# Performance work log

Measured on AMD Instinct MI355X. Metric: run time of the kernel, lower is better.

Reference implementation:

```python
import jax, jax.numpy as jnp
import numpy as np

N = 100000   # nodes
E = 1600000  # edges
D = 128      # input / hidden feature dim
H = 16       # inner GCN bottleneck (gin default hidden_filters=(16,))
C = 40       # num_classes (ogbn-arxiv)
L = 3        # GCN2 layers
EPS = 1e-5   # hk.BatchNorm default eps


def setup_inputs() -> dict:
    key = jax.random.key(0)
    ks = jax.random.split(key, 8)
    x = jax.random.normal(ks[0], (N, D), jnp.float32)
    vals = jax.random.uniform(ks[1], (E,), jnp.float32)
    row = jnp.sort(jax.random.randint(ks[2], (E,), 0, N, jnp.int32))
    col = jax.random.randint(ks[3], (E,), 0, N, jnp.int32)
    W1 = jax.random.normal(ks[4], (L, D, H), jnp.float32) * 0.1
    b1 = jnp.zeros((L, H), jnp.float32)
    W2 = jax.random.normal(ks[5], (L, H, D), jnp.float32) * 0.1
    b2 = jnp.zeros((L, D), jnp.float32)
    gamma = jnp.ones((L, D), jnp.float32)
    beta = jnp.zeros((L, D), jnp.float32)
    W1f = jax.random.normal(ks[6], (D, H), jnp.float32) * 0.1
    b1f = jnp.zeros((H,), jnp.float32)
    W2f = jax.random.normal(ks[7], (H, C), jnp.float32) * 0.1
    b2f = jnp.zeros((C,), jnp.float32)
    return dict(x=x, vals=vals, W1=W1, b1=b1, W2=W2, b2=b2, gamma=gamma,
                beta=beta, W1f=W1f, b1f=b1f, W2f=W2f, b2f=b2f, row=row, col=col)


def spmm(row, col, vals, h):
    # out[i] = sum_{e: row[e]==i} vals[e] * h[col[e]]  (A @ h, A sparse COO)
    return jax.ops.segment_sum(vals[:, None] * h[col], row,
                               num_segments=N, indices_are_sorted=True)


def gcn_block(x, row, col, vals, w1, c1, w2, c2):
    # inner GCN: GraphConv(16) -> relu -> GraphConv(out); dropout_rate=0 -> identity
    h = spmm(row, col, vals, x @ w1) + c1
    h = jax.nn.relu(h)
    return spmm(row, col, vals, h @ w2) + c2


def reference(x, vals, W1, b1, W2, b2, gamma, beta, W1f, b1f, W2f, b2f, row, col):
    for i in range(L):
        h = gcn_block(x, row, col, vals, W1[i], b1[i], W2[i], b2[i])
        # BatchNorm (training mode: batch stats over node axis)
        mean = jnp.mean(h, axis=0)
        var = jnp.mean(jnp.square(h), axis=0) - jnp.square(mean)
        h = (h - mean) * jax.lax.rsqrt(var + EPS) * gamma[i] + beta[i]
        x = jax.nn.relu(h)
    logits = gcn_block(x, row, col, vals, W1f, b1f, W2f, b2f)
    return logits
```

## Files before the change

kernel.cpp:

```cpp
#include <hip/hip_runtime.h>

#define NN 100000
#define NE 1600000
#define DD 128
#define HH 16
#define CC 40
#define LL 3

typedef int   vi4 __attribute__((ext_vector_type(4)));
typedef float vf4 __attribute__((ext_vector_type(4)));

__device__ __forceinline__ float4 f4fma(float s, float4 w, float4 a) {
    a.x = fmaf(s, w.x, a.x); a.y = fmaf(s, w.y, a.y);
    a.z = fmaf(s, w.z, a.z); a.w = fmaf(s, w.w, a.w);
    return a;
}

__device__ __forceinline__ unsigned short f2bf(float f) {
    unsigned u = __float_as_uint(f);
    unsigned r = u + 0x7fffu + ((u >> 16) & 1u);
    return (unsigned short)(r >> 16);
}
__device__ __forceinline__ unsigned pk2(float a, float b) {
    return (unsigned)f2bf(a) | ((unsigned)f2bf(b) << 16);
}
__device__ __forceinline__ float bflo(unsigned u) { return __uint_as_float(u << 16); }
__device__ __forceinline__ float bfhi(unsigned u) { return __uint_as_float(u & 0xffff0000u); }

__device__ __forceinline__ int permW2(int dw) {
    return (dw >> 2) | ((dw & 3) << 3);
}

__global__ void build_rowptr(const int* __restrict__ row, int* __restrict__ rp) {
    int e = blockIdx.x * 256 + threadIdx.x;
    if (e >= NE) return;
    int r1 = row[e];
    int r0 = (e == 0) ? -1 : row[e - 1];
    for (int i = r0 + 1; i <= r1; i++) rp[i] = e;
    if (e == NE - 1) {
        for (int i = r1 + 1; i <= NN; i++) rp[i] = NE;
    }
}

__global__ void zero_buf(float* __restrict__ s, int n) {
    int i = blockIdx.x * 256 + threadIdx.x;
    if (i < n) s[i] = 0.f;
}

__launch_bounds__(256)
__global__ void gemm_dh_reg(const float* __restrict__ X, const float* __restrict__ W,
                            unsigned* __restrict__ Y) {
    __shared__ float4 Ws[DD * 4];
    int t = threadIdx.x;
    for (int i = t; i < DD * 4; i += 256) Ws[i] = ((const float4*)W)[i];
    __syncthreads();
    int n = blockIdx.x * 256 + t;
    if (n >= NN) return;
    const float4* X4 = (const float4*)(X + (size_t)n * DD);
    float4 y0 = {0,0,0,0}, y1 = {0,0,0,0}, y2 = {0,0,0,0}, y3 = {0,0,0,0};
    #pragma unroll 8
    for (int dc = 0; dc < 32; dc++) {
        float4 xv = X4[dc];
        float xs[4] = {xv.x, xv.y, xv.z, xv.w};
        #pragma unroll
        for (int j = 0; j < 4; j++) {
            int d = dc * 4 + j;
            float xj = xs[j];
            y0 = f4fma(xj, Ws[d * 4 + 0], y0);
            y1 = f4fma(xj, Ws[d * 4 + 1], y1);
            y2 = f4fma(xj, Ws[d * 4 + 2], y2);
            y3 = f4fma(xj, Ws[d * 4 + 3], y3);
        }
    }
    uint4 o0 = {pk2(y0.x, y0.y), pk2(y0.z, y0.w), pk2(y1.x, y1.y), pk2(y1.z, y1.w)};
    uint4 o1 = {pk2(y2.x, y2.y), pk2(y2.z, y2.w), pk2(y3.x, y3.y), pk2(y3.z, y3.w)};
    ((uint4*)Y)[(size_t)n * 2]     = o0;
    ((uint4*)Y)[(size_t)n * 2 + 1] = o1;
}

#define FMA_B(vv, g0, g1, g2, g3)                                                      \
    acc.x = fmaf(vv.x, bflo(g0.x), acc.x); acc.y = fmaf(vv.x, bfhi(g0.x), acc.y);      \
    acc.z = fmaf(vv.x, bflo(g0.y), acc.z); acc.w = fmaf(vv.x, bfhi(g0.y), acc.w);      \
    acc.x = fmaf(vv.y, bflo(g1.x), acc.x); acc.y = fmaf(vv.y, bfhi(g1.x), acc.y);      \
    acc.z = fmaf(vv.y, bflo(g1.y), acc.z); acc.w = fmaf(vv.y, bfhi(g1.y), acc.w);      \
    acc.x = fmaf(vv.z, bflo(g2.x), acc.x); acc.y = fmaf(vv.z, bfhi(g2.x), acc.y);      \
    acc.z = fmaf(vv.z, bflo(g2.y), acc.z); acc.w = fmaf(vv.z, bfhi(g2.y), acc.w);      \
    acc.x = fmaf(vv.w, bflo(g3.x), acc.x); acc.y = fmaf(vv.w, bfhi(g3.x), acc.y);      \
    acc.z = fmaf(vv.w, bflo(g3.y), acc.z); acc.w = fmaf(vv.w, bfhi(g3.y), acc.w);

template <bool RELU, bool BIAS, bool OBF, bool GRAM>
__launch_bounds__(256)
__global__ void spmm16(const int* __restrict__ rp, const int* __restrict__ col,
                       const float* __restrict__ vals, const unsigned* __restrict__ hin,
                       const float* __restrict__ bias, void* __restrict__ outv,
                       float* __restrict__ GS) {
    int node = blockIdx.x * 64 + (threadIdx.x >> 2);
    int f = threadIdx.x & 3;
    bool valid = node < NN;
    if (!GRAM && !valid) return;
    float4 acc = {0, 0, 0, 0};
    if (valid) {
        int s = rp[node], e = rp[node + 1];
        const uint2* h2 = (const uint2*)hin;
        int j = s;
        int sa = min((s + 3) & ~3, e);
        for (; j < sa; j++) {
            uint2 g = h2[(size_t)col[j] * 4 + f];
            float v = vals[j];
            acc.x = fmaf(v, bflo(g.x), acc.x); acc.y = fmaf(v, bfhi(g.x), acc.y);
            acc.z = fmaf(v, bflo(g.y), acc.z); acc.w = fmaf(v, bfhi(g.y), acc.w);
        }
        int nb = (e - j) >> 2;
        if (nb >= 2) {
            vi4 cA = __builtin_nontemporal_load((const vi4*)(col + j));
            vf4 vA = __builtin_nontemporal_load((const vf4*)(vals + j));
            vi4 cB = __builtin_nontemporal_load((const vi4*)(col + j + 4));
            vf4 vB = __builtin_nontemporal_load((const vf4*)(vals + j + 4));
            uint2 gA0 = h2[(size_t)cA.x * 4 + f];
            uint2 gA1 = h2[(size_t)cA.y * 4 + f];
            uint2 gA2 = h2[(size_t)cA.z * 4 + f];
            uint2 gA3 = h2[(size_t)cA.w * 4 + f];
            int jj = j + 8;
            j += nb << 2;
            for (int r = nb - 2; r > 0; r--) {
                vi4 cC = __builtin_nontemporal_load((const vi4*)(col + jj));
                vf4 vC = __builtin_nontemporal_load((const vf4*)(vals + jj));
                uint2 gB0 = h2[(size_t)cB.x * 4 + f];
                uint2 gB1 = h2[(size_t)cB.y * 4 + f];
                uint2 gB2 = h2[(size_t)cB.z * 4 + f];
                uint2 gB3 = h2[(size_t)cB.w * 4 + f];
                FMA_B(vA, gA0, gA1, gA2, gA3)
                vA = vB; vB = vC; cB = cC;
                gA0 = gB0; gA1 = gB1; gA2 = gB2; gA3 = gB3;
                jj += 4;
            }
            uint2 gB0 = h2[(size_t)cB.x * 4 + f];
            uint2 gB1 = h2[(size_t)cB.y * 4 + f];
            uint2 gB2 = h2[(size_t)cB.z * 4 + f];
            uint2 gB3 = h2[(size_t)cB.w * 4 + f];
            FMA_B(vA, gA0, gA1, gA2, gA3)
            FMA_B(vB, gB0, gB1, gB2, gB3)
        } else if (nb == 1) {
            vi4 cA = __builtin_nontemporal_load((const vi4*)(col + j));
            vf4 vA = __builtin_nontemporal_load((const vf4*)(vals + j));
            uint2 gA0 = h2[(size_t)cA.x * 4 + f];
            uint2 gA1 = h2[(size_t)cA.y * 4 + f];
            uint2 gA2 = h2[(size_t)cA.z * 4 + f];
            uint2 gA3 = h2[(size_t)cA.w * 4 + f];
            FMA_B(vA, gA0, gA1, gA2, gA3)
            j += 4;
        }
        for (; j < e; j++) {
            uint2 g = h2[(size_t)col[j] * 4 + f];
            float v = vals[j];
            acc.x = fmaf(v, bflo(g.x), acc.x); acc.y = fmaf(v, bfhi(g.x), acc.y);
            acc.z = fmaf(v, bflo(g.y), acc.z); acc.w = fmaf(v, bfhi(g.y), acc.w);
        }
        if (BIAS) {
            float4 b = ((const float4*)bias)[f];
            acc.x += b.x; acc.y += b.y; acc.z += b.z; acc.w += b.w;
        }
        if (RELU) {
            acc.x = fmaxf(acc.x, 0.f); acc.y = fmaxf(acc.y, 0.f);
            acc.z = fmaxf(acc.z, 0.f); acc.w = fmaxf(acc.w, 0.f);
        }
        if (OBF) {
            uint2 o = {pk2(acc.x, acc.y), pk2(acc.z, acc.w)};
            ((uint2*)outv)[(size_t)node * 4 + f] = o;
        } else {
            ((float4*)outv)[(size_t)node * 4 + f] = acc;
        }
    }
    if (GRAM) {
        __shared__ float Us[64 * 20];
        int nl = threadIdx.x >> 2;
        float4 z = valid ? acc : (float4){0, 0, 0, 0};
        ((float4*)&Us[nl * 20])[f] = z;
        __syncthreads();
        int k = threadIdx.x & 15, kp = threadIdx.x >> 4;
        float g = 0.f, s = 0.f;
        for (int n = 0; n < 64; n++) {
            float a = Us[n * 20 + k];
            float b = Us[n * 20 + kp];
            g = fmaf(a, b, g);
            s += a;
        }
        float* gs = GS + (blockIdx.x & 7) * 272;
        atomicAdd(&gs[kp * 16 + k], g);
        if (kp == 0) atomicAdd(&gs[256 + k], s);
    }
}

__launch_bounds__(128)
__global__ void bn_prep(const float* __restrict__ GS, const float* __restrict__ W2,
                        const float* __restrict__ b2, const float* __restrict__ gamma,
                        const float* __restrict__ beta, float* __restrict__ SCSH) {
    __shared__ float Gs[272];
    int t = threadIdx.x;
    for (int i = t; i < 272; i += 128) {
        float a = 0.f;
        #pragma unroll
        for (int c = 0; c < 8; c++) a += GS[c * 272 + i];
        Gs[i] = a;
    }
    __syncthreads();
    int d = t;
    float w[16];
    #pragma unroll
    for (int k = 0; k < 16; k++) w[k] = W2[k * DD + d];
    float sdot = 0.f, quad = 0.f;
    #pragma unroll
    for (int k = 0; k < 16; k++) {
        sdot = fmaf(Gs[256 + k], w[k], sdot);
        float vk = 0.f;
        #pragma unroll
        for (int kp = 0; kp < 16; kp++) vk = fmaf(Gs[k * 16 + kp], w[kp], vk);
        quad = fmaf(w[k], vk, quad);
    }
    float b = b2[d];
    float sumH  = sdot + (float)NN * b;
    float sumsq = quad + 2.f * b * sdot + (float)NN * b * b;
    float mean = sumH * (1.f / NN);
    float var  = sumsq * (1.f / NN) - mean * mean;
    float inv  = rsqrtf(var + 1e-5f);
    float gm = gamma[d] * inv;
    SCSH[d] = gm;
    SCSH[128 + d] = (b - mean) * gm + beta[d];
}

__launch_bounds__(256)
__global__ void fused_mid(const float* __restrict__ U, const float* __restrict__ SCSH,
                          const float* __restrict__ W2, const float* __restrict__ W1n,
                          unsigned* __restrict__ Y) {
    __shared__ float4 W2s[HH * 32];
    __shared__ float4 W1s[DD * 4];
    __shared__ float4 SC4[32], SH4[32];
    int t = threadIdx.x;
    for (int i = t; i < HH * 32; i += 256) {
        int k = i >> 5, dw = i & 31;
        W2s[k * 32 + permW2(dw)] = ((const float4*)W2)[i];
    }
    for (int i = t; i < DD * 4; i += 256) {
        int d = i >> 2, q = i & 3;
        W1s[d * 4 + ((q + (d >> 4)) & 3)] = ((const float4*)W1n)[i];
    }
    if (t < 32) SC4[permW2(t)] = ((const float4*)SCSH)[t];
    else if (t < 64) SH4[permW2(t - 32)] = ((const float4*)SCSH)[t];
    __syncthreads();
    int g = t >> 3, p = t & 7;
    int base = blockIdx.x * 64;
    int n[2]; bool v[2];
    #pragma unroll
    for (int i = 0; i < 2; i++) { n[i] = base + i * 32 + g; v[i] = n[i] < NN; }
    float u[2][16];
    #pragma unroll
    for (int i = 0; i < 2; i++) {
        if (v[i]) {
            const float4* up = (const float4*)(U + (size_t)n[i] * HH);
            float4 a = up[0], b = up[1], c = up[2], d = up[3];
            u[i][0]=a.x; u[i][1]=a.y; u[i][2]=a.z; u[i][3]=a.w;
            u[i][4]=b.x; u[i][5]=b.y; u[i][6]=b.z; u[i][7]=b.w;
            u[i][8]=c.x; u[i][9]=c.y; u[i][10]=c.z; u[i][11]=c.w;
            u[i][12]=d.x; u[i][13]=d.y; u[i][14]=d.z; u[i][15]=d.w;
        } else {
            #pragma unroll
            for (int k = 0; k < 16; k++) u[i][k] = 0.f;
        }
    }
    float4 y[2][4];
    #pragma unroll
    for (int i = 0; i < 2; i++)
        #pragma unroll
        for (int q = 0; q < 4; q++) y[i][q] = {0, 0, 0, 0};
    #pragma unroll
    for (int dqi = 0; dqi < 4; dqi++) {
        int rpos = p + (dqi << 3);
        float4 h[2] = {{0,0,0,0},{0,0,0,0}};
        #pragma unroll
        for (int k = 0; k < 16; k++) {
            float4 w = W2s[k * 32 + rpos];
            h[0] = f4fma(u[0][k], w, h[0]);
            h[1] = f4fma(u[1][k], w, h[1]);
        }
        float4 s4 = SC4[rpos], t4 = SH4[rpos];
        #pragma unroll
        for (int i = 0; i < 2; i++) {
            h[i].x = fmaxf(fmaf(h[i].x, s4.x, t4.x), 0.f);
            h[i].y = fmaxf(fmaf(h[i].y, s4.y, t4.y), 0.f);
            h[i].z = fmaxf(fmaf(h[i].z, s4.z, t4.z), 0.f);
            h[i].w = fmaxf(fmaf(h[i].w, s4.w, t4.w), 0.f);
        }
        int dq = (p << 2) + dqi;
        #pragma unroll
        for (int j = 0; j < 4; j++) {
            int d = (dq << 2) + j;
            float4 w0 = W1s[d * 4 + ((0 + p) & 3)];
            float4 w1 = W1s[d * 4 + ((1 + p) & 3)];
            float4 w2 = W1s[d * 4 + ((2 + p) & 3)];
            float4 w3 = W1s[d * 4 + ((3 + p) & 3)];
            float h0 = j == 0 ? h[0].x : j == 1 ? h[0].y : j == 2 ? h[0].z : h[0].w;
            float h1 = j == 0 ? h[1].x : j == 1 ? h[1].y : j == 2 ? h[1].z : h[1].w;
            y[0][0] = f4fma(h0, w0, y[0][0]); y[0][1] = f4fma(h0, w1, y[0][1]);
            y[0][2] = f4fma(h0, w2, y[0][2]); y[0][3] = f4fma(h0, w3, y[0][3]);
            y[1][0] = f4fma(h1, w0, y[1][0]); y[1][1] = f4fma(h1, w1, y[1][1]);
            y[1][2] = f4fma(h1, w2, y[1][2]); y[1][3] = f4fma(h1, w3, y[1][3]);
        }
    }
    float4 ar[4];
    #pragma unroll
    for (int q = 0; q < 4; q++) {
        float4 z0 = y[0][q], z1 = y[1][q];
        z0.x += __shfl_xor(z0.x, 4); z0.y += __shfl_xor(z0.y, 4);
        z0.z += __shfl_xor(z0.z, 4); z0.w += __shfl_xor(z0.w, 4);
        z1.x += __shfl_xor(z1.x, 4); z1.y += __shfl_xor(z1.y, 4);
        z1.z += __shfl_xor(z1.z, 4); z1.w += __shfl_xor(z1.w, 4);
        ar[q].x = (p & 4) ? z1.x : z0.x;
        ar[q].y = (p & 4) ? z1.y : z0.y;
        ar[q].z = (p & 4) ? z1.z : z0.z;
        ar[q].w = (p & 4) ? z1.w : z0.w;
    }
    float4 br[2];
    #pragma unroll
    for (int q = 0; q < 2; q++) {
        float4 z0 = ar[q], z1 = ar[2 + q];
        z0.x += __shfl_xor(z0.x, 2); z0.y += __shfl_xor(z0.y, 2);
        z0.z += __shfl_xor(z0.z, 2); z0.w += __shfl_xor(z0.w, 2);
        z1.x += __shfl_xor(z1.x, 2); z1.y += __shfl_xor(z1.y, 2);
        z1.z += __shfl_xor(z1.z, 2); z1.w += __shfl_xor(z1.w, 2);
        br[q].x = (p & 2) ? z1.x : z0.x;
        br[q].y = (p & 2) ? z1.y : z0.y;
        br[q].z = (p & 2) ? z1.z : z0.z;
        br[q].w = (p & 2) ? z1.w : z0.w;
    }
    float4 c;
    {
        float4 z0 = br[0], z1 = br[1];
        z0.x += __shfl_xor(z0.x, 1); z0.y += __shfl_xor(z0.y, 1);
        z0.z += __shfl_xor(z0.z, 1); z0.w += __shfl_xor(z0.w, 1);
        z1.x += __shfl_xor(z1.x, 1); z1.y += __shfl_xor(z1.y, 1);
        z1.z += __shfl_xor(z1.z, 1); z1.w += __shfl_xor(z1.w, 1);
        c.x = (p & 1) ? z1.x : z0.x;
        c.y = (p & 1) ? z1.y : z0.y;
        c.z = (p & 1) ? z1.z : z0.z;
        c.w = (p & 1) ? z1.w : z0.w;
    }
    bool vv = (p & 4) ? v[1] : v[0];
    int  nn = (p & 4) ? n[1] : n[0];
    int  q  = p & 3;
    if (vv) {
        uint2 o = {pk2(c.x, c.y), pk2(c.z, c.w)};
        ((uint2*)Y)[(size_t)nn * 4 + q] = o;
    }
}

__launch_bounds__(256)
__global__ void gemm_hc_reg(const float* __restrict__ U, const float* __restrict__ W,
                            const float* __restrict__ bias, float* __restrict__ out) {
    __shared__ float2 Ws[HH * 20];
    __shared__ float2 Bs[20];
    int t = threadIdx.x;
    for (int i = t; i < HH * 20; i += 256) Ws[i] = ((const float2*)W)[i];
    if (t < 20) Bs[t] = ((const float2*)bias)[t];
    __syncthreads();
    int node = blockIdx.x * 64 + (t >> 2);
    int p = t & 3;
    if (node >= NN) return;
    float u[16];
    {
        const float4* up = (const float4*)(U + (size_t)node * HH);
        float4 a = up[0], b = up[1], c = up[2], d = up[3];
        u[0]=a.x; u[1]=a.y; u[2]=a.z; u[3]=a.w; u[4]=b.x; u[5]=b.y; u[6]=b.z; u[7]=b.w;
        u[8]=c.x; u[9]=c.y; u[10]=c.z; u[11]=c.w; u[12]=d.x; u[13]=d.y; u[14]=d.z; u[15]=d.w;
    }
    float2 acc[5];
    #pragma unroll
    for (int i = 0; i < 5; i++) acc[i] = Bs[p * 5 + i];
    #pragma unroll
    for (int k = 0; k < 16; k++) {
        float uk = u[k];
        #pragma unroll
        for (int i = 0; i < 5; i++) {
            float2 w = Ws[k * 20 + p * 5 + i];
            acc[i].x = fmaf(uk, w.x, acc[i].x);
            acc[i].y = fmaf(uk, w.y, acc[i].y);
        }
    }
    float2* O = (float2*)(out + (size_t)node * CC) + p * 5;
    #pragma unroll
    for (int i = 0; i < 5; i++) O[i] = acc[i];
}

extern "C" void kernel_launch(void* const* d_in, const int* in_sizes, int n_in,
                              void* d_out, int out_size, void* d_ws, size_t ws_size,
                              hipStream_t stream) {
    const float* x     = (const float*)d_in[0];
    const float* vals  = (const float*)d_in[1];
    const float* W1    = (const float*)d_in[2];
    const float* b1    = (const float*)d_in[3];
    const float* W2    = (const float*)d_in[4];
    const float* b2    = (const float*)d_in[5];
    const float* gamma = (const float*)d_in[6];
    const float* beta  = (const float*)d_in[7];
    const float* W1f   = (const float*)d_in[8];
    const float* b1f   = (const float*)d_in[9];
    const float* W2f   = (const float*)d_in[10];
    const float* b2f   = (const float*)d_in[11];
    const int*   row   = (const int*)d_in[12];
    const int*   col   = (const int*)d_in[13];
    float* out = (float*)d_out;

    char* ws = (char*)d_ws;
    size_t off = 0;
    auto alloc = [&](size_t bytes) -> char* {
        char* p = ws + off;
        off += (bytes + 255) / 256 * 256;
        return p;
    };
    int*      rp   = (int*)     alloc((NN + 1) * sizeof(int));
    float*    GSC  = (float*)   alloc((size_t)LL * 8 * 272 * sizeof(float));
    float*    SCSH = (float*)   alloc(256 * sizeof(float));
    unsigned* Yb   = (unsigned*)alloc((size_t)NN * HH * 2);
    unsigned* Tb   = (unsigned*)alloc((size_t)NN * HH * 2);
    float*    U    = (float*)   alloc((size_t)NN * HH * sizeof(float));

    build_rowptr<<<(NE + 255) / 256, 256, 0, stream>>>(row, rp);
    zero_buf<<<(LL * 8 * 272 + 255) / 256, 256, 0, stream>>>(GSC, LL * 8 * 272);

    gemm_dh_reg<<<(NN + 255) / 256, 256, 0, stream>>>(x, W1, Yb);
    for (int l = 0; l < LL; l++) {
        spmm16<true, true, true, false><<<(NN + 63) / 64, 256, 0, stream>>>(
            rp, col, vals, Yb, b1 + l * HH, Tb, nullptr);
        spmm16<false, false, false, true><<<(NN + 63) / 64, 256, 0, stream>>>(
            rp, col, vals, Tb, nullptr, U, GSC + (size_t)l * 8 * 272);
        bn_prep<<<1, 128, 0, stream>>>(GSC + (size_t)l * 8 * 272, W2 + l * HH * DD,
                                       b2 + l * DD, gamma + l * DD, beta + l * DD, SCSH);
        const float* W1next = (l < LL - 1) ? (W1 + (l + 1) * DD * HH) : W1f;
        fused_mid<<<(NN + 63) / 64, 256, 0, stream>>>(U, SCSH, W2 + l * HH * DD, W1next, Yb);
    }
    spmm16<true, true, true, false><<<(NN + 63) / 64, 256, 0, stream>>>(
        rp, col, vals, Yb, b1f, Tb, nullptr);
    spmm16<false, false, false, false><<<(NN + 63) / 64, 256, 0, stream>>>(
        rp, col, vals, Tb, nullptr, U, nullptr);
    gemm_hc_reg<<<(NN + 63) / 64, 256, 0, stream>>>(U, W2f, b2f, out);
}
```

Before: 416.7 us.

## Fuse final HxC projection into last SpMM and restructure gather loop with masked blocks

The last SpMM now computes the 16-to-40 output projection in-block through shared memory, which removes the separate gemm_hc_reg kernel and the U round-trip to global memory. The SpMM inner loop is rewritten to process aligned 4-edge blocks with masked values and a three-deep prefetch, instead of using scalar head and tail loops. The aim is to reduce branch overhead and increase memory-level parallelism. In exchange it issues some wasted gathers on the masked lanes and drops the nontemporal loads.

```diff
diff --git a/kernel.cpp b/kernel.cpp
--- a/kernel.cpp
+++ b/kernel.cpp
@@ -88,73 +88,65 @@
     acc.x = fmaf(vv.w, bflo(g3.x), acc.x); acc.y = fmaf(vv.w, bfhi(g3.x), acc.y);      \
     acc.z = fmaf(vv.w, bflo(g3.y), acc.z); acc.w = fmaf(vv.w, bfhi(g3.y), acc.w);
 
-template <bool RELU, bool BIAS, bool OBF, bool GRAM>
+__device__ __forceinline__ void ldc(const int* __restrict__ col,
+                                    const float* __restrict__ vals,
+                                    int jb, int s, int e, vi4& c, vf4& v) {
+    c = *(const vi4*)(col + jb);
+    vf4 w = *(const vf4*)(vals + jb);
+    int r = jb - s;
+    unsigned deg = (unsigned)(e - s);
+    v.x = ((unsigned)(r + 0) < deg) ? w.x : 0.f;
+    v.y = ((unsigned)(r + 1) < deg) ? w.y : 0.f;
+    v.z = ((unsigned)(r + 2) < deg) ? w.z : 0.f;
+    v.w = ((unsigned)(r + 3) < deg) ? w.w : 0.f;
+}
+
+template <bool RELU, bool BIAS, bool OBF, bool GRAM, bool FINAL>
 __launch_bounds__(256)
 __global__ void spmm16(const int* __restrict__ rp, const int* __restrict__ col,
                        const float* __restrict__ vals, const unsigned* __restrict__ hin,
                        const float* __restrict__ bias, void* __restrict__ outv,
-                       float* __restrict__ GS) {
+                       float* __restrict__ GS, const float* __restrict__ Wf,
+                       const float* __restrict__ bf, float* __restrict__ outc) {
+    __shared__ float2 Wc[FINAL ? HH * 20 : 1];
+    __shared__ float2 Bc[FINAL ? 20 : 1];
+    if (FINAL) {
+        for (int i = threadIdx.x; i < HH * 20; i += 256) Wc[i] = ((const float2*)Wf)[i];
+        if (threadIdx.x < 20) Bc[threadIdx.x] = ((const float2*)bf)[threadIdx.x];
+    }
     int node = blockIdx.x * 64 + (threadIdx.x >> 2);
     int f = threadIdx.x & 3;
     bool valid = node < NN;
-    if (!GRAM && !valid) return;
+    if (!GRAM && !FINAL && !valid) return;
     float4 acc = {0, 0, 0, 0};
     if (valid) {
         int s = rp[node], e = rp[node + 1];
         const uint2* h2 = (const uint2*)hin;
-        int j = s;
-        int sa = min((s + 3) & ~3, e);
-        for (; j < sa; j++) {
-            uint2 g = h2[(size_t)col[j] * 4 + f];
-            float v = vals[j];
-            acc.x = fmaf(v, bflo(g.x), acc.x); acc.y = fmaf(v, bfhi(g.x), acc.y);
-            acc.z = fmaf(v, bflo(g.y), acc.z); acc.w = fmaf(v, bfhi(g.y), acc.w);
-        }
-        int nb = (e - j) >> 2;
-        if (nb >= 2) {
-            vi4 cA = __builtin_nontemporal_load((const vi4*)(col + j));
-            vf4 vA = __builtin_nontemporal_load((const vf4*)(vals + j));
-            vi4 cB = __builtin_nontemporal_load((const vi4*)(col + j + 4));
-            vf4 vB = __builtin_nontemporal_load((const vf4*)(vals + j + 4));
-            uint2 gA0 = h2[(size_t)cA.x * 4 + f];
-            uint2 gA1 = h2[(size_t)cA.y * 4 + f];
-            uint2 gA2 = h2[(size_t)cA.z * 4 + f];
-            uint2 gA3 = h2[(size_t)cA.w * 4 + f];
-            int jj = j + 8;
-            j += nb << 2;
-            for (int r = nb - 2; r > 0; r--) {
-                vi4 cC = __builtin_nontemporal_load((const vi4*)(col + jj));
-                vf4 vC = __builtin_nontemporal_load((const vf4*)(vals + jj));
-                uint2 gB0 = h2[(size_t)cB.x * 4 + f];
-                uint2 gB1 = h2[(size_t)cB.y * 4 + f];
-                uint2 gB2 = h2[(size_t)cB.z * 4 + f];
-                uint2 gB3 = h2[(size_t)cB.w * 4 + f];
-                FMA_B(vA, gA0, gA1, gA2, gA3)
-                vA = vB; vB = vC; cB = cC;
+        int deg = e - s;
+        if (deg > 0) {
+            int s0 = s & ~3;
+            int B = (e - s0 + 3) >> 2;
+            vi4 c2, c0, c1; vf4 v0, v1, v2;
+            ldc(col, vals, s0, s, e, c0, v0);
+            if (B > 1) ldc(col, vals, s0 + 4, s, e, c1, v1);
+            else { c1 = c0; v1 = (vf4){0, 0, 0, 0}; }
+            if (B > 2) ldc(col, vals, s0 + 8, s, e, c2, v2);
+            else { c2 = c1; v2 = (vf4){0, 0, 0, 0}; }
+            uint2 gA0 = h2[(size_t)c0.x * 4 + f], gA1 = h2[(size_t)c0.y * 4 + f];
+            uint2 gA2 = h2[(size_t)c0.z * 4 + f], gA3 = h2[(size_t)c0.w * 4 + f];
+            uint2 gB0 = h2[(size_t)c1.x * 4 + f], gB1 = h2[(size_t)c1.y * 4 + f];
+            uint2 gB2 = h2[(size_t)c1.z * 4 + f], gB3 = h2[(size_t)c1.w * 4 + f];
+            for (int b = 0; b < B; b++) {
+                vi4 c3; vf4 v3;
+                if (b + 3 < B) ldc(col, vals, s0 + ((b + 3) << 2), s, e, c3, v3);
+                else { c3 = c2; v3 = (vf4){0, 0, 0, 0}; }
+                uint2 gC0 = h2[(size_t)c2.x * 4 + f], gC1 = h2[(size_t)c2.y * 4 + f];
+                uint2 gC2 = h2[(size_t)c2.z * 4 + f], gC3 = h2[(size_t)c2.w * 4 + f];
+                FMA_B(v0, gA0, gA1, gA2, gA3)
+                v0 = v1; v1 = v2; v2 = v3; c2 = c3;
                 gA0 = gB0; gA1 = gB1; gA2 = gB2; gA3 = gB3;
-                jj += 4;
+                gB0 = gC0; gB1 = gC1; gB2 = gC2; gB3 = gC3;
             }
-            uint2 gB0 = h2[(size_t)cB.x * 4 + f];
-            uint2 gB1 = h2[(size_t)cB.y * 4 + f];
-            uint2 gB2 = h2[(size_t)cB.z * 4 + f];
-            uint2 gB3 = h2[(size_t)cB.w * 4 + f];
-            FMA_B(vA, gA0, gA1, gA2, gA3)
-            FMA_B(vB, gB0, gB1, gB2, gB3)
-        } else if (nb == 1) {
-            vi4 cA = __builtin_nontemporal_load((const vi4*)(col + j));
-            vf4 vA = __builtin_nontemporal_load((const vf4*)(vals + j));
-            uint2 gA0 = h2[(size_t)cA.x * 4 + f];
-            uint2 gA1 = h2[(size_t)cA.y * 4 + f];
-            uint2 gA2 = h2[(size_t)cA.z * 4 + f];
-            uint2 gA3 = h2[(size_t)cA.w * 4 + f];
-            FMA_B(vA, gA0, gA1, gA2, gA3)
-            j += 4;
-        }
-        for (; j < e; j++) {
-            uint2 g = h2[(size_t)col[j] * 4 + f];
-            float v = vals[j];
-            acc.x = fmaf(v, bflo(g.x), acc.x); acc.y = fmaf(v, bfhi(g.x), acc.y);
-            acc.z = fmaf(v, bflo(g.y), acc.z); acc.w = fmaf(v, bfhi(g.y), acc.w);
         }
         if (BIAS) {
             float4 b = ((const float4*)bias)[f];
@@ -164,11 +156,13 @@
             acc.x = fmaxf(acc.x, 0.f); acc.y = fmaxf(acc.y, 0.f);
             acc.z = fmaxf(acc.z, 0.f); acc.w = fmaxf(acc.w, 0.f);
         }
-        if (OBF) {
-            uint2 o = {pk2(acc.x, acc.y), pk2(acc.z, acc.w)};
-            ((uint2*)outv)[(size_t)node * 4 + f] = o;
-        } else {
-            ((float4*)outv)[(size_t)node * 4 + f] = acc;
+        if (!FINAL) {
+            if (OBF) {
+                uint2 o = {pk2(acc.x, acc.y), pk2(acc.z, acc.w)};
+                ((uint2*)outv)[(size_t)node * 4 + f] = o;
+            } else {
+                ((float4*)outv)[(size_t)node * 4 + f] = acc;
+            }
         }
     }
     if (GRAM) {
@@ -189,6 +183,35 @@
         atomicAdd(&gs[kp * 16 + k], g);
         if (kp == 0) atomicAdd(&gs[256 + k], s);
     }
+    if (FINAL) {
+        __shared__ float Us[64 * 20];
+        int nl = threadIdx.x >> 2;
+        ((float4*)&Us[nl * 20])[f] = acc;
+        __syncthreads();
+        int p = threadIdx.x & 3;
+        int onode = blockIdx.x * 64 + (threadIdx.x >> 2);
+        if (onode < NN) {
+            float u[16];
+            #pragma unroll
+            for (int k = 0; k < 16; k++) u[k] = Us[(threadIdx.x >> 2) * 20 + k];
+            float2 a5[5];
+            #pragma unroll
+            for (int i = 0; i < 5; i++) a5[i] = Bc[p * 5 + i];
+            #pragma unroll
+            for (int k = 0; k < 16; k++) {
+                float uk = u[k];
+                #pragma unroll
+                for (int i = 0; i < 5; i++) {
+                    float2 w = Wc[k * 20 + p * 5 + i];
+                    a5[i].x = fmaf(uk, w.x, a5[i].x);
+                    a5[i].y = fmaf(uk, w.y, a5[i].y);
+                }
+            }
+            float2* O = (float2*)(outc + (size_t)onode * CC) + p * 5;
+            #pragma unroll
+            for (int i = 0; i < 5; i++) O[i] = a5[i];
+        }
+    }
 }
 
 __launch_bounds__(128)
@@ -351,43 +374,6 @@
         uint2 o = {pk2(c.x, c.y), pk2(c.z, c.w)};
         ((uint2*)Y)[(size_t)nn * 4 + q] = o;
     }
-}
-
-__launch_bounds__(256)
-__global__ void gemm_hc_reg(const float* __restrict__ U, const float* __restrict__ W,
-                            const float* __restrict__ bias, float* __restrict__ out) {
-    __shared__ float2 Ws[HH * 20];
-    __shared__ float2 Bs[20];
-    int t = threadIdx.x;
-    for (int i = t; i < HH * 20; i += 256) Ws[i] = ((const float2*)W)[i];
-    if (t < 20) Bs[t] = ((const float2*)bias)[t];
-    __syncthreads();
-    int node = blockIdx.x * 64 + (t >> 2);
-    int p = t & 3;
-    if (node >= NN) return;
-    float u[16];
-    {
-        const float4* up = (const float4*)(U + (size_t)node * HH);
-        float4 a = up[0], b = up[1], c = up[2], d = up[3];
-        u[0]=a.x; u[1]=a.y; u[2]=a.z; u[3]=a.w; u[4]=b.x; u[5]=b.y; u[6]=b.z; u[7]=b.w;
-        u[8]=c.x; u[9]=c.y; u[10]=c.z; u[11]=c.w; u[12]=d.x; u[13]=d.y; u[14]=d.z; u[15]=d.w;
-    }
-    float2 acc[5];
-    #pragma unroll
-    for (int i = 0; i < 5; i++) acc[i] = Bs[p * 5 + i];
-    #pragma unroll
-    for (int k = 0; k < 16; k++) {
-        float uk = u[k];
-        #pragma unroll
-        for (int i = 0; i < 5; i++) {
-            float2 w = Ws[k * 20 + p * 5 + i];
-            acc[i].x = fmaf(uk, w.x, acc[i].x);
-            acc[i].y = fmaf(uk, w.y, acc[i].y);
-        }
-    }
-    float2* O = (float2*)(out + (size_t)node * CC) + p * 5;
-    #pragma unroll
-    for (int i = 0; i < 5; i++) O[i] = acc[i];
 }
 
 extern "C" void kernel_launch(void* const* d_in, const int* in_sizes, int n_in,
@@ -428,18 +414,17 @@
 
     gemm_dh_reg<<<(NN + 255) / 256, 256, 0, stream>>>(x, W1, Yb);
     for (int l = 0; l < LL; l++) {
-        spmm16<true, true, true, false><<<(NN + 63) / 64, 256, 0, stream>>>(
-            rp, col, vals, Yb, b1 + l * HH, Tb, nullptr);
-        spmm16<false, false, false, true><<<(NN + 63) / 64, 256, 0, stream>>>(
-            rp, col, vals, Tb, nullptr, U, GSC + (size_t)l * 8 * 272);
+        spmm16<true, true, true, false, false><<<(NN + 63) / 64, 256, 0, stream>>>(
+            rp, col, vals, Yb, b1 + l * HH, Tb, nullptr, nullptr, nullptr, nullptr);
+        spmm16<false, false, false, true, false><<<(NN + 63) / 64, 256, 0, stream>>>(
+            rp, col, vals, Tb, nullptr, U, GSC + (size_t)l * 8 * 272, nullptr, nullptr, nullptr);
         bn_prep<<<1, 128, 0, stream>>>(GSC + (size_t)l * 8 * 272, W2 + l * HH * DD,
                                        b2 + l * DD, gamma + l * DD, beta + l * DD, SCSH);
         const float* W1next = (l < LL - 1) ? (W1 + (l + 1) * DD * HH) : W1f;
         fused_mid<<<(NN + 63) / 64, 256, 0, stream>>>(U, SCSH, W2 + l * HH * DD, W1next, Yb);
     }
-    spmm16<true, true, true, false><<<(NN + 63) / 64, 256, 0, stream>>>(
-        rp, col, vals, Yb, b1f, Tb, nullptr);
-    spmm16<false, false, false, false><<<(NN + 63) / 64, 256, 0, stream>>>(
-        rp, col, vals, Tb, nullptr, U, nullptr);
-    gemm_hc_reg<<<(NN + 63) / 64, 256, 0, stream>>>(U, W2f, b2f, out);
-}
+    spmm16<true, true, true, false, false><<<(NN + 63) / 64, 256, 0, stream>>>(
+        rp, col, vals, Yb, b1f, Tb, nullptr, nullptr, nullptr, nullptr);
+    spmm16<false, false, false, false, true><<<(NN + 63) / 64, 256, 0, stream>>>(
+        rp, col, vals, Tb, nullptr, nullptr, nullptr, W2f, b2f, out);
+}
```

Result: faster. 370.5 us (-11.1%).
